# Performance work log

Measured on AMD Instinct MI355X. Metric: run time of the kernel, lower is better.

## Reference

```python
import jax, jax.numpy as jnp
import numpy as np

CON_SIZE = 1024  # num_gz; used in the 1/sqrt(con_size) score scaling


def setup_inputs() -> dict:
    key = jax.random.key(0)
    k1, k2, k3, k4, k5 = jax.random.split(key, 5)
    B, K, D, P = 1024, 256, 1024, 768
    return {
        "joint_feature": jax.random.normal(k1, (B, D), dtype=jnp.float32),
        "confounder_dictionary": jax.random.normal(k2, (K, D), dtype=jnp.float32),
        "prior": jax.random.uniform(k3, (K, 1), dtype=jnp.float32),
        "Wq": jax.random.normal(k4, (D, P), dtype=jnp.float32) * (1.0 / np.sqrt(D)),
        "Wk": jax.random.normal(k5, (D, P), dtype=jnp.float32) * (1.0 / np.sqrt(D)),
    }


def reference(joint_feature, confounder_dictionary, prior, Wq, Wk):
    # dot_product_intervention
    q = joint_feature @ Wq                       # [B, 768]
    k = confounder_dictionary @ Wk               # [K, 768]
    scores = (q @ k.T) * (1.0 / jnp.sqrt(jnp.float32(CON_SIZE)))  # [B, K]
    attn = jax.nn.softmax(scores, axis=-1)       # softmax over confounders
    # (attn[b,k,1] * conf[k,d] * prior[k,1]).sum(1)  == attn @ (conf * prior)
    g_z = jnp.einsum('bk,kd->bd', attn, confounder_dictionary * prior)  # [B, D]
    return joint_feature + g_z
```

## Files before the change

kernel.cpp:

```cpp
#include <hip/hip_runtime.h>
#include <hip/hip_bf16.h>


typedef __attribute__((ext_vector_type(8))) short short8;
typedef __attribute__((ext_vector_type(4))) float f32x4;

__device__ __forceinline__ ushort f2bf(float x) {
    union { float f; uint u; } c; c.f = x;
    return (ushort)((c.u + 0x7FFFu + ((c.u >> 16) & 1u)) >> 16);
}
__device__ __forceinline__ float bflo(uint u) {
    union { uint u; float f; } c; c.u = u << 16; return c.f;
}
__device__ __forceinline__ float bfhi(uint u) {
    union { uint u; float f; } c; c.u = u & 0xFFFF0000u; return c.f;
}

__global__ __launch_bounds__(256)
void prep_kernel(const float* __restrict__ J, const float* __restrict__ conf,
                 const float* __restrict__ prior, const float* __restrict__ Wq,
                 const float* __restrict__ Wk,
                 ushort* __restrict__ Jb, ushort* __restrict__ confb,
                 ushort* __restrict__ WqT, ushort* __restrict__ WkT,
                 ushort* __restrict__ cpT)
{
    const int t = threadIdx.x;
    int b = blockIdx.x;

    if (b < 1280) {
        const float* src; ushort* dst; int base;
        if (b < 1024) { src = J;    dst = Jb;    base = b * 1024; }
        else          { src = conf; dst = confb; base = (b - 1024) * 1024; }
        const float4 v = *(const float4*)(src + base + t * 4);
        ushort4 o;
        o.x = f2bf(v.x); o.y = f2bf(v.y); o.z = f2bf(v.z); o.w = f2bf(v.w);
        *(ushort4*)(dst + base + t * 4) = o;
        return;
    }

    __shared__ float tile[32][33];
    const float* src; ushort* dst; int R, C, tpr; bool usePrior;
    if (b < 2048)      { b -= 1280; src = Wq;   dst = WqT; R = 1024; C = 768;  tpr = 24; usePrior = false; }
    else if (b < 2816) { b -= 2048; src = Wk;   dst = WkT; R = 1024; C = 768;  tpr = 24; usePrior = false; }
    else               { b -= 2816; src = conf; dst = cpT; R = 256;  C = 1024; tpr = 32; usePrior = true;  }
    const int rt = b / tpr, ct = b % tpr;

    {
        const int row = t >> 3, c4 = (t & 7) << 2;
        const float4 v = *(const float4*)(src + (size_t)(rt * 32 + row) * C + ct * 32 + c4);
        const float p = usePrior ? prior[rt * 32 + row] : 1.0f;
        tile[row][c4 + 0] = v.x * p; tile[row][c4 + 1] = v.y * p;
        tile[row][c4 + 2] = v.z * p; tile[row][c4 + 3] = v.w * p;
    }
    __syncthreads();
    {
        const int orow = t >> 3, oc4 = (t & 7) << 2;
        ushort4 o;
        o.x = f2bf(tile[oc4 + 0][orow]); o.y = f2bf(tile[oc4 + 1][orow]);
        o.z = f2bf(tile[oc4 + 2][orow]); o.w = f2bf(tile[oc4 + 3][orow]);
        *(ushort4*)(dst + (size_t)(ct * 32 + orow) * R + rt * 32 + oc4) = o;
    }
}

__global__ __launch_bounds__(512)
void qk_kernel(const ushort* __restrict__ Jb, const ushort* __restrict__ WqT,
               const ushort* __restrict__ confb, const ushort* __restrict__ WkT,
               ushort* __restrict__ qb, ushort* __restrict__ kmb)
{
    __shared__ __align__(16) ushort As[64][72];
    __shared__ __align__(16) ushort Bs[64][72];

    int bid = blockIdx.x;
    const ushort *A, *B; ushort* C;
    if (bid < 192) { A = Jb; B = WqT; C = qb; }
    else           { bid -= 192; A = confb; B = WkT; C = kmb; }
    const int m0 = (bid / 12) * 64, n0 = (bid % 12) * 64;
    const int N = 768, K = 1024;

    const int t = threadIdx.x;
    const int wave = t >> 6, lane = t & 63;
    const int wm = (wave >> 1) * 16;
    const int wn = (wave & 1) * 32;
    const int lrow = lane & 15, lko = (lane >> 4) * 8;

    f32x4 acc0 = (f32x4)0.0f, acc1 = (f32x4)0.0f;

    const int sr = t >> 3, sk = (t & 7) << 3;
    const ushort* Ap = A + (size_t)(m0 + sr) * K + sk;
    const ushort* Bp = B + (size_t)(n0 + sr) * K + sk;
    uint4 av = *(const uint4*)(Ap);
    uint4 bv = *(const uint4*)(Bp);

    for (int k0 = 0; k0 < K; k0 += 64) {
        *(uint4*)&As[sr][sk] = av;
        *(uint4*)&Bs[sr][sk] = bv;
        __syncthreads();
        if (k0 + 64 < K) {
            av = *(const uint4*)(Ap + k0 + 64);
            bv = *(const uint4*)(Bp + k0 + 64);
        }
        #pragma unroll
        for (int kk = 0; kk < 64; kk += 32) {
            const short8 a  = *(const short8*)&As[wm + lrow][kk + lko];
            const short8 b0 = *(const short8*)&Bs[wn + lrow][kk + lko];
            const short8 b1 = *(const short8*)&Bs[wn + 16 + lrow][kk + lko];
            acc0 = __builtin_amdgcn_mfma_f32_16x16x32_bf16(a, b0, acc0, 0, 0, 0);
            acc1 = __builtin_amdgcn_mfma_f32_16x16x32_bf16(a, b1, acc1, 0, 0, 0);
        }
        __syncthreads();
    }

    const int quad = lane >> 4;
    #pragma unroll
    for (int j = 0; j < 2; ++j) {
        const f32x4 acc = j ? acc1 : acc0;
        #pragma unroll
        for (int r = 0; r < 4; ++r) {
            const int m = m0 + wm + quad * 4 + r;
            const int n = n0 + wn + j * 16 + lrow;
            C[(size_t)m * N + n] = f2bf(acc[r]);
        }
    }
}

__global__ __launch_bounds__(256)
void scores_kernel(const ushort* __restrict__ qb, const ushort* __restrict__ kmb,
                   ushort* __restrict__ sc)
{
    __shared__ __align__(16) ushort As[32][72];
    __shared__ __align__(16) ushort Bs[32][72];

    const int m0 = blockIdx.y * 32, n0 = blockIdx.x * 32;
    const int t = threadIdx.x;
    const int wave = t >> 6, lane = t & 63;
    const int wm = (wave >> 1) * 16, wn = (wave & 1) * 16;
    const int lrow = lane & 15, lko = (lane >> 4) * 8;

    f32x4 acc = (f32x4)0.0f;

    const int sr = t >> 3, sk = (t & 7) << 3;
    const ushort* Ap = qb  + (size_t)(m0 + sr) * 768 + sk;
    const ushort* Bp = kmb + (size_t)(n0 + sr) * 768 + sk;
    uint4 av = *(const uint4*)(Ap);
    uint4 bv = *(const uint4*)(Bp);

    for (int k0 = 0; k0 < 768; k0 += 64) {
        *(uint4*)&As[sr][sk] = av;
        *(uint4*)&Bs[sr][sk] = bv;
        __syncthreads();
        if (k0 + 64 < 768) {
            av = *(const uint4*)(Ap + k0 + 64);
            bv = *(const uint4*)(Bp + k0 + 64);
        }
        #pragma unroll
        for (int kk = 0; kk < 64; kk += 32) {
            const short8 a = *(const short8*)&As[wm + lrow][kk + lko];
            const short8 b = *(const short8*)&Bs[wn + lrow][kk + lko];
            acc = __builtin_amdgcn_mfma_f32_16x16x32_bf16(a, b, acc, 0, 0, 0);
        }
        __syncthreads();
    }

    const int quad = lane >> 4;
    #pragma unroll
    for (int r = 0; r < 4; ++r) {
        const int m = m0 + wm + quad * 4 + r;
        const int n = n0 + wn + lrow;
        sc[(size_t)m * 256 + n] = f2bf(acc[r] * 0.03125f);
    }
}

__global__ __launch_bounds__(256)
void out_kernel(const ushort* __restrict__ sc, const ushort* __restrict__ cpT,
                const float* __restrict__ J, float* __restrict__ out)
{
    __shared__ __align__(16) ushort At[64][264];
    __shared__ __align__(16) ushort Bs[64][72];
    __shared__ float rowInv[64];

    const int t = threadIdx.x;
    const int m0 = blockIdx.y * 64, n0 = blockIdx.x * 64;

    {
        const int row = t >> 2;
        const int cb  = (t & 3) * 64;
        const ushort* srow = sc + (size_t)(m0 + row) * 256 + cb;
        uint4 s[8];
        #pragma unroll
        for (int i = 0; i < 8; ++i) s[i] = *(const uint4*)(srow + i * 8);

        float mx = -1e30f;
        #pragma unroll
        for (int i = 0; i < 8; ++i) {
            mx = fmaxf(mx, fmaxf(fmaxf(bflo(s[i].x), bfhi(s[i].x)),
                                 fmaxf(bflo(s[i].y), bfhi(s[i].y))));
            mx = fmaxf(mx, fmaxf(fmaxf(bflo(s[i].z), bfhi(s[i].z)),
                                 fmaxf(bflo(s[i].w), bfhi(s[i].w))));
        }
        mx = fmaxf(mx, __shfl_xor(mx, 1));
        mx = fmaxf(mx, __shfl_xor(mx, 2));

        float sum = 0.0f;
        #pragma unroll
        for (int i = 0; i < 8; ++i) {
            uint4 o;
            uint* su = (uint*)&s[i];
            uint* ou = (uint*)&o;
            #pragma unroll
            for (int w = 0; w < 4; ++w) {
                const ushort e0 = f2bf(__expf(bflo(su[w]) - mx));
                const ushort e1 = f2bf(__expf(bfhi(su[w]) - mx));
                sum += bflo((uint)e0) + bflo((uint)e1);
                ou[w] = (uint)e0 | ((uint)e1 << 16);
            }
            *(uint4*)&At[row][cb + i * 8] = o;
        }
        sum += __shfl_xor(sum, 1);
        sum += __shfl_xor(sum, 2);
        if ((t & 3) == 0) rowInv[row] = 1.0f / sum;
    }
    __syncthreads();

    const int wave = t >> 6, lane = t & 63;
    const int wm = (wave >> 1) * 32, wn = (wave & 1) * 32;
    const int lrow = lane & 15, lko = (lane >> 4) * 8;

    f32x4 acc[2][2];
    #pragma unroll
    for (int i = 0; i < 2; ++i)
        #pragma unroll
        for (int j = 0; j < 2; ++j) acc[i][j] = (f32x4)0.0f;

    const int sr = t >> 2, sk = (t & 3) << 4;
    const ushort* Bp = cpT + (size_t)(n0 + sr) * 256 + sk;
    uint4 bv0 = *(const uint4*)(Bp);
    uint4 bv1 = *(const uint4*)(Bp + 8);

    for (int k0 = 0; k0 < 256; k0 += 64) {
        *(uint4*)&Bs[sr][sk]     = bv0;
        *(uint4*)&Bs[sr][sk + 8] = bv1;
        __syncthreads();
        if (k0 + 64 < 256) {
            bv0 = *(const uint4*)(Bp + k0 + 64);
            bv1 = *(const uint4*)(Bp + k0 + 72);
        }
        #pragma unroll
        for (int kk = 0; kk < 64; kk += 32) {
            const short8 a0 = *(const short8*)&At[wm + lrow][k0 + kk + lko];
            const short8 a1 = *(const short8*)&At[wm + 16 + lrow][k0 + kk + lko];
            const short8 b0 = *(const short8*)&Bs[wn + lrow][kk + lko];
            const short8 b1 = *(const short8*)&Bs[wn + 16 + lrow][kk + lko];
            acc[0][0] = __builtin_amdgcn_mfma_f32_16x16x32_bf16(a0, b0, acc[0][0], 0, 0, 0);
            acc[0][1] = __builtin_amdgcn_mfma_f32_16x16x32_bf16(a0, b1, acc[0][1], 0, 0, 0);
            acc[1][0] = __builtin_amdgcn_mfma_f32_16x16x32_bf16(a1, b0, acc[1][0], 0, 0, 0);
            acc[1][1] = __builtin_amdgcn_mfma_f32_16x16x32_bf16(a1, b1, acc[1][1], 0, 0, 0);
        }
        __syncthreads();
    }

    const int quad = lane >> 4;
    #pragma unroll
    for (int i = 0; i < 2; ++i)
        #pragma unroll
        for (int j = 0; j < 2; ++j)
            #pragma unroll
            for (int r = 0; r < 4; ++r) {
                const int mrel = wm + i * 16 + quad * 4 + r;
                const int m = m0 + mrel;
                const int n = n0 + wn + j * 16 + lrow;
                const size_t off = (size_t)m * 1024 + n;
                out[off] = acc[i][j][r] * rowInv[mrel] + J[off];
            }
}

extern "C" void kernel_launch(void* const* d_in, const int* in_sizes, int n_in,
                              void* d_out, int out_size, void* d_ws, size_t ws_size,
                              hipStream_t stream)
{
    const float* J     = (const float*)d_in[0];
    const float* conf  = (const float*)d_in[1];
    const float* prior = (const float*)d_in[2];
    const float* Wq    = (const float*)d_in[3];
    const float* Wk    = (const float*)d_in[4];
    float* out = (float*)d_out;

    ushort* ws = (ushort*)d_ws;
    ushort* Jb    = ws;
    ushort* confb = Jb    + 1048576;
    ushort* WqT   = confb + 262144;
    ushort* WkT   = WqT   + 786432;
    ushort* cpT   = WkT   + 786432;
    ushort* qb    = cpT   + 262144;
    ushort* kmb   = qb    + 786432;
    ushort* scb   = kmb   + 196608;

    prep_kernel<<<3072, 256, 0, stream>>>(J, conf, prior, Wq, Wk,
                                          Jb, confb, WqT, WkT, cpT);
    qk_kernel<<<240, 512, 0, stream>>>(Jb, WqT, confb, WkT, qb, kmb);
    scores_kernel<<<dim3(8, 32), 256, 0, stream>>>(qb, kmb, scb);
    out_kernel<<<dim3(16, 16), 256, 0, stream>>>(scb, cpT, J, out);
}
```

Baseline: 92.10 us.

## Use direct global-to-LDS loads with XOR-swizzled double buffering in GEMM kernels

Replaces the register-staged global loads plus LDS stores in qk, scores and out kernels with global_load_lds direct-to-LDS transfers into double-buffered tiles. Rows are stored unpadded with an XOR swizzle on 16-byte chunks to avoid bank conflicts, and each iteration issues the next tile's loads before computing on the current one. This removes the VGPR round-trip and one barrier per iteration, at the cost of a full vmcnt(0) drain each step and doubled LDS for the B and A tiles.

```diff
diff --git a/kernel.cpp b/kernel.cpp
--- a/kernel.cpp
+++ b/kernel.cpp
@@ -14,6 +14,17 @@
 }
 __device__ __forceinline__ float bfhi(uint u) {
     union { uint u; float f; } c; c.u = u & 0xFFFF0000u; return c.f;
+}
+
+__device__ __forceinline__ void gload16(const ushort* g, ushort* l) {
+    __builtin_amdgcn_global_load_lds(
+        (const __attribute__((address_space(1))) void*)g,
+        (__attribute__((address_space(3))) void*)l, 16, 0, 0);
+}
+#define DRAIN() do { asm volatile("s_waitcnt vmcnt(0)" ::: "memory"); __syncthreads(); } while (0)
+
+__device__ __forceinline__ short8 ldsfrag(const ushort* flat, int row, int g) {
+    return *(const short8*)(flat + (row << 6) + (((g ^ (row & 7)) << 3)));
 }
 
 __global__ __launch_bounds__(256)
@@ -67,8 +78,8 @@
                const ushort* __restrict__ confb, const ushort* __restrict__ WkT,
                ushort* __restrict__ qb, ushort* __restrict__ kmb)
 {
-    __shared__ __align__(16) ushort As[64][72];
-    __shared__ __align__(16) ushort Bs[64][72];
+    __shared__ __align__(16) ushort As[2][64 * 64];
+    __shared__ __align__(16) ushort Bs[2][64 * 64];
 
     int bid = blockIdx.x;
     const ushort *A, *B; ushort* C;
@@ -81,33 +92,38 @@
     const int wave = t >> 6, lane = t & 63;
     const int wm = (wave >> 1) * 16;
     const int wn = (wave & 1) * 32;
-    const int lrow = lane & 15, lko = (lane >> 4) * 8;
+    const int lrow = lane & 15, g0 = lane >> 4;
+
+    const int r = lane >> 3, c = lane & 7;
+    const ushort* Ag = A + (size_t)(m0 + 8 * wave + r) * K + ((c ^ r) << 3);
+    const ushort* Bg = B + (size_t)(n0 + 8 * wave + r) * K + ((c ^ r) << 3);
+    const int lbase = wave * 512;
 
     f32x4 acc0 = (f32x4)0.0f, acc1 = (f32x4)0.0f;
 
-    const int sr = t >> 3, sk = (t & 7) << 3;
-    const ushort* Ap = A + (size_t)(m0 + sr) * K + sk;
-    const ushort* Bp = B + (size_t)(n0 + sr) * K + sk;
-    uint4 av = *(const uint4*)(Ap);
-    uint4 bv = *(const uint4*)(Bp);
-
+    gload16(Ag, &As[0][lbase]);
+    gload16(Bg, &Bs[0][lbase]);
+    DRAIN();
+
+    int cur = 0;
     for (int k0 = 0; k0 < K; k0 += 64) {
-        *(uint4*)&As[sr][sk] = av;
-        *(uint4*)&Bs[sr][sk] = bv;
-        __syncthreads();
         if (k0 + 64 < K) {
-            av = *(const uint4*)(Ap + k0 + 64);
-            bv = *(const uint4*)(Bp + k0 + 64);
-        }
-        #pragma unroll
-        for (int kk = 0; kk < 64; kk += 32) {
-            const short8 a  = *(const short8*)&As[wm + lrow][kk + lko];
-            const short8 b0 = *(const short8*)&Bs[wn + lrow][kk + lko];
-            const short8 b1 = *(const short8*)&Bs[wn + 16 + lrow][kk + lko];
+            gload16(Ag + k0 + 64, &As[cur ^ 1][lbase]);
+            gload16(Bg + k0 + 64, &Bs[cur ^ 1][lbase]);
+        }
+        const ushort* Af = As[cur];
+        const ushort* Bf = Bs[cur];
+        #pragma unroll
+        for (int kk = 0; kk < 2; ++kk) {
+            const int g = (kk << 2) + g0;
+            const short8 a  = ldsfrag(Af, wm + lrow, g);
+            const short8 b0 = ldsfrag(Bf, wn + lrow, g);
+            const short8 b1 = ldsfrag(Bf, wn + 16 + lrow, g);
             acc0 = __builtin_amdgcn_mfma_f32_16x16x32_bf16(a, b0, acc0, 0, 0, 0);
             acc1 = __builtin_amdgcn_mfma_f32_16x16x32_bf16(a, b1, acc1, 0, 0, 0);
         }
-        __syncthreads();
+        DRAIN();
+        cur ^= 1;
     }
 
     const int quad = lane >> 4;
@@ -115,10 +131,10 @@
     for (int j = 0; j < 2; ++j) {
         const f32x4 acc = j ? acc1 : acc0;
         #pragma unroll
-        for (int r = 0; r < 4; ++r) {
-            const int m = m0 + wm + quad * 4 + r;
+        for (int rr = 0; rr < 4; ++rr) {
+            const int m = m0 + wm + quad * 4 + rr;
             const int n = n0 + wn + j * 16 + lrow;
-            C[(size_t)m * N + n] = f2bf(acc[r]);
+            C[(size_t)m * N + n] = f2bf(acc[rr]);
         }
     }
 }
@@ -127,46 +143,51 @@
 void scores_kernel(const ushort* __restrict__ qb, const ushort* __restrict__ kmb,
                    ushort* __restrict__ sc)
 {
-    __shared__ __align__(16) ushort As[32][72];
-    __shared__ __align__(16) ushort Bs[32][72];
+    __shared__ __align__(16) ushort As[2][32 * 64];
+    __shared__ __align__(16) ushort Bs[2][32 * 64];
 
     const int m0 = blockIdx.y * 32, n0 = blockIdx.x * 32;
     const int t = threadIdx.x;
     const int wave = t >> 6, lane = t & 63;
     const int wm = (wave >> 1) * 16, wn = (wave & 1) * 16;
-    const int lrow = lane & 15, lko = (lane >> 4) * 8;
+    const int lrow = lane & 15, g0 = lane >> 4;
+
+    const int r = lane >> 3, c = lane & 7;
+    const ushort* Ag = qb  + (size_t)(m0 + 8 * wave + r) * 768 + ((c ^ r) << 3);
+    const ushort* Bg = kmb + (size_t)(n0 + 8 * wave + r) * 768 + ((c ^ r) << 3);
+    const int lbase = wave * 512;
 
     f32x4 acc = (f32x4)0.0f;
 
-    const int sr = t >> 3, sk = (t & 7) << 3;
-    const ushort* Ap = qb  + (size_t)(m0 + sr) * 768 + sk;
-    const ushort* Bp = kmb + (size_t)(n0 + sr) * 768 + sk;
-    uint4 av = *(const uint4*)(Ap);
-    uint4 bv = *(const uint4*)(Bp);
-
+    gload16(Ag, &As[0][lbase]);
+    gload16(Bg, &Bs[0][lbase]);
+    DRAIN();
+
+    int cur = 0;
     for (int k0 = 0; k0 < 768; k0 += 64) {
-        *(uint4*)&As[sr][sk] = av;
-        *(uint4*)&Bs[sr][sk] = bv;
-        __syncthreads();
         if (k0 + 64 < 768) {
-            av = *(const uint4*)(Ap + k0 + 64);
-            bv = *(const uint4*)(Bp + k0 + 64);
-        }
-        #pragma unroll
-        for (int kk = 0; kk < 64; kk += 32) {
-            const short8 a = *(const short8*)&As[wm + lrow][kk + lko];
-            const short8 b = *(const short8*)&Bs[wn + lrow][kk + lko];
+            gload16(Ag + k0 + 64, &As[cur ^ 1][lbase]);
+            gload16(Bg + k0 + 64, &Bs[cur ^ 1][lbase]);
+        }
+        const ushort* Af = As[cur];
+        const ushort* Bf = Bs[cur];
+        #pragma unroll
+        for (int kk = 0; kk < 2; ++kk) {
+            const int g = (kk << 2) + g0;
+            const short8 a = ldsfrag(Af, wm + lrow, g);
+            const short8 b = ldsfrag(Bf, wn + lrow, g);
             acc = __builtin_amdgcn_mfma_f32_16x16x32_bf16(a, b, acc, 0, 0, 0);
         }
-        __syncthreads();
+        DRAIN();
+        cur ^= 1;
     }
 
     const int quad = lane >> 4;
     #pragma unroll
-    for (int r = 0; r < 4; ++r) {
-        const int m = m0 + wm + quad * 4 + r;
+    for (int rr = 0; rr < 4; ++rr) {
+        const int m = m0 + wm + quad * 4 + rr;
         const int n = n0 + wn + lrow;
-        sc[(size_t)m * 256 + n] = f2bf(acc[r] * 0.03125f);
+        sc[(size_t)m * 256 + n] = f2bf(acc[rr] * 0.03125f);
     }
 }
 
@@ -175,11 +196,19 @@
                 const float* __restrict__ J, float* __restrict__ out)
 {
     __shared__ __align__(16) ushort At[64][264];
-    __shared__ __align__(16) ushort Bs[64][72];
+    __shared__ __align__(16) ushort Bs[2][64 * 64];
     __shared__ float rowInv[64];
 
     const int t = threadIdx.x;
     const int m0 = blockIdx.y * 64, n0 = blockIdx.x * 64;
+    const int wave = t >> 6, lane = t & 63;
+
+    const int r = lane >> 3, c = lane & 7;
+    const ushort* Bg = cpT + (size_t)(n0 + 16 * wave + r) * 256 + ((c ^ r) << 3);
+    const int lbase = wave * 1024;
+
+    gload16(Bg,            &Bs[0][lbase]);
+    gload16(Bg + 8 * 256,  &Bs[0][lbase + 512]);
 
     {
         const int row = t >> 2;
@@ -219,11 +248,10 @@
         sum += __shfl_xor(sum, 2);
         if ((t & 3) == 0) rowInv[row] = 1.0f / sum;
     }
-    __syncthreads();
-
-    const int wave = t >> 6, lane = t & 63;
+    DRAIN();
+
     const int wm = (wave >> 1) * 32, wn = (wave & 1) * 32;
-    const int lrow = lane & 15, lko = (lane >> 4) * 8;
+    const int lrow = lane & 15, lko = (lane >> 4) * 8, g0 = lane >> 4;
 
     f32x4 acc[2][2];
     #pragma unroll
@@ -231,31 +259,27 @@
         #pragma unroll
         for (int j = 0; j < 2; ++j) acc[i][j] = (f32x4)0.0f;
 
-    const int sr = t >> 2, sk = (t & 3) << 4;
-    const ushort* Bp = cpT + (size_t)(n0 + sr) * 256 + sk;
-    uint4 bv0 = *(const uint4*)(Bp);
-    uint4 bv1 = *(const uint4*)(Bp + 8);
-
+    int cur = 0;
     for (int k0 = 0; k0 < 256; k0 += 64) {
-        *(uint4*)&Bs[sr][sk]     = bv0;
-        *(uint4*)&Bs[sr][sk + 8] = bv1;
-        __syncthreads();
         if (k0 + 64 < 256) {
-            bv0 = *(const uint4*)(Bp + k0 + 64);
-            bv1 = *(const uint4*)(Bp + k0 + 72);
-        }
+            gload16(Bg + k0 + 64,           &Bs[cur ^ 1][lbase]);
+            gload16(Bg + 8 * 256 + k0 + 64, &Bs[cur ^ 1][lbase + 512]);
+        }
+        const ushort* Bf = Bs[cur];
         #pragma unroll
         for (int kk = 0; kk < 64; kk += 32) {
+            const int g = (kk >> 3) + g0;
             const short8 a0 = *(const short8*)&At[wm + lrow][k0 + kk + lko];
             const short8 a1 = *(const short8*)&At[wm + 16 + lrow][k0 + kk + lko];
-            const short8 b0 = *(const short8*)&Bs[wn + lrow][kk + lko];
-            const short8 b1 = *(const short8*)&Bs[wn + 16 + lrow][kk + lko];
+            const short8 b0 = ldsfrag(Bf, wn + lrow, g);
+            const short8 b1 = ldsfrag(Bf, wn + 16 + lrow, g);
             acc[0][0] = __builtin_amdgcn_mfma_f32_16x16x32_bf16(a0, b0, acc[0][0], 0, 0, 0);
             acc[0][1] = __builtin_amdgcn_mfma_f32_16x16x32_bf16(a0, b1, acc[0][1], 0, 0, 0);
             acc[1][0] = __builtin_amdgcn_mfma_f32_16x16x32_bf16(a1, b0, acc[1][0], 0, 0, 0);
             acc[1][1] = __builtin_amdgcn_mfma_f32_16x16x32_bf16(a1, b1, acc[1][1], 0, 0, 0);
         }
-        __syncthreads();
+        DRAIN();
+        cur ^= 1;
     }
 
     const int quad = lane >> 4;
@@ -264,12 +288,12 @@
         #pragma unroll
         for (int j = 0; j < 2; ++j)
             #pragma unroll
-            for (int r = 0; r < 4; ++r) {
-                const int mrel = wm + i * 16 + quad * 4 + r;
+            for (int rr = 0; rr < 4; ++rr) {
+                const int mrel = wm + i * 16 + quad * 4 + rr;
                 const int m = m0 + mrel;
                 const int n = n0 + wn + j * 16 + lrow;
                 const size_t off = (size_t)m * 1024 + n;
-                out[off] = acc[i][j][r] * rowInv[mrel] + J[off];
+                out[off] = acc[i][j][rr] * rowInv[mrel] + J[off];
             }
 }
 
```

Result: slower. 99.10 us (+7.6%).
